# Optimization experiments

Measured on AMD Instinct MI355X. Metric: run time of the kernel, lower is better.

The kernel has to match this reference:

```python
import jax, jax.numpy as jnp
import numpy as np
from jax import lax

C = 512
B, T, N = 8, 16, 32
KSZ = 7
NEG_SLOPE = 0.01
LN_EPS = 1e-5


def setup_inputs() -> dict:
    key = jax.random.key(0)
    ks = jax.random.split(key, 8)
    local_feat = jax.random.normal(ks[0], (B, T, N, C), dtype=jnp.float32)
    global_feat = jax.random.normal(ks[1], (B, C), dtype=jnp.float32)
    pos = jax.random.normal(ks[2], (B, T, N, 3), dtype=jnp.float32)
    # adj_weight: nn.Linear(C, C, bias=False), init eye_ (perturb slightly to keep interesting ties)
    W = jnp.eye(C, dtype=jnp.float32) + 0.01 * jax.random.normal(ks[3], (C, C), dtype=jnp.float32)
    # depthwise Conv1d(C, C, 7, groups=C): weight [C, 1, 7], kaiming init; bias zeros
    conv_w = jax.random.normal(ks[4], (C, 1, KSZ), dtype=jnp.float32) * np.sqrt(2.0 / KSZ)
    conv_b = jnp.zeros((C,), dtype=jnp.float32)
    ln_gamma = jnp.ones((C,), dtype=jnp.float32)
    ln_beta = jnp.zeros((C,), dtype=jnp.float32)
    return {"local_feat": local_feat, "global_feat": global_feat, "pos": pos,
            "W": W, "conv_w": conv_w, "conv_b": conv_b,
            "ln_gamma": ln_gamma, "ln_beta": ln_beta}


def reference(local_feat, global_feat, pos, W, conv_w, conv_b, ln_gamma, ln_beta):
    b, t, nd, c = local_feat.shape
    n = t * nd
    feat = local_feat.reshape(b, n, c)
    # F.normalize(p=2, dim=-1, eps=1e-12)
    norm = feat / jnp.maximum(jnp.linalg.norm(feat, axis=-1, keepdims=True), 1e-12)
    # torch.einsum('bnc,cc,bcm->bnm'): repeated 'cc' takes the diagonal of W
    A = jnp.einsum('bnc,cc,bcm->bnm', norm, W, jnp.swapaxes(norm, 1, 2))
    A = A.reshape(b, n, t, nd)
    top_A = jnp.argmax(A, axis=-1)  # [b, n, t]
    # direct indexed gather -- avoids the [b, n, t, nd, c] stacked blowup
    top_feat = local_feat[jnp.arange(b)[:, None, None],
                          jnp.arange(t)[None, None, :],
                          top_A]                                 # [b, n, t, c]
    x = jnp.swapaxes(top_feat.reshape(b * n, t, c), 1, 2)        # [b*n, c, t]
    # depthwise conv1d, kernel 7, valid padding
    y = lax.conv_general_dilated(x, conv_w, window_strides=(1,), padding='VALID',
                                 dimension_numbers=('NCH', 'OIH', 'NCH'),
                                 feature_group_count=c)
    y = y + conv_b[None, :, None]                                # [b*n, c, t-6]
    y = jnp.swapaxes(y, 1, 2)                                    # [b*n, t-6, c]
    mu = jnp.mean(y, axis=-1, keepdims=True)
    var = jnp.mean(jnp.square(y - mu), axis=-1, keepdims=True)
    ln = (y - mu) * lax.rsqrt(var + LN_EPS) * ln_gamma + ln_beta
    act = jnp.where(ln >= 0, ln, NEG_SLOPE * ln)
    out = jnp.mean(act, axis=1)                                  # mean over time -> [b*n, c]
    return out.reshape(b, t, nd, c)
```

## Files before the change

### kernel.cpp

```cpp
#include <hip/hip_runtime.h>
#include <hip/hip_bf16.h>

#define C_DIM 512
#define B_DIM 8
#define T_DIM 16
#define ND_DIM 32
#define NPTS 512
#define ROWS 4096
#define KSZ 7
#define TOUT 10
#define NEG_SLOPE 0.01f
#define LN_EPS 1e-5f

__global__ __launch_bounds__(256) void norm_kernel(const float* __restrict__ feat,
                                                   float* __restrict__ nrm) {
    int row = blockIdx.x;
    int tid = threadIdx.x;
    const float* f = feat + (size_t)row * C_DIM;
    float* o = nrm + (size_t)row * C_DIM;
    float v0 = f[tid];
    float v1 = f[tid + 256];
    float ss = v0 * v0 + v1 * v1;
    #pragma unroll
    for (int off = 32; off > 0; off >>= 1) ss += __shfl_down(ss, off, 64);
    __shared__ float wsum[4];
    int wid = tid >> 6, lane = tid & 63;
    if (lane == 0) wsum[wid] = ss;
    __syncthreads();
    float tot = wsum[0] + wsum[1] + wsum[2] + wsum[3];
    float inv = 1.0f / fmaxf(sqrtf(tot), 1e-12f);
    o[tid] = v0 * inv;
    o[tid + 256] = v1 * inv;
}

__global__ __launch_bounds__(256) void gemm_argmax_kernel(const float* __restrict__ nrm,
                                                          const float* __restrict__ W,
                                                          int* __restrict__ idxg) {
    __shared__ __align__(16) float As[16][68];
    __shared__ __align__(16) float Bs[16][68];
    __shared__ float Cs[64][65];
    __shared__ float wd[C_DIM];
    const int tid = threadIdx.x;
    const int tx = tid & 15, ty = tid >> 4;
    const int b = blockIdx.z;
    const int row0 = blockIdx.y * 64, col0 = blockIdx.x * 64;
    const float* Nb = nrm + (size_t)b * NPTS * C_DIM;

    wd[tid]       = W[(size_t)tid * (C_DIM + 1)];
    wd[tid + 256] = W[(size_t)(tid + 256) * (C_DIM + 1)];
    __syncthreads();

    float acc[4][4] = {};
    for (int k0 = 0; k0 < C_DIM; k0 += 16) {
        #pragma unroll
        for (int e = 0; e < 4; e++) {
            int idx = tid + e * 256;
            int m = idx >> 4, kk = idx & 15;
            As[kk][m] = Nb[(size_t)(row0 + m) * C_DIM + k0 + kk] * wd[k0 + kk];
            Bs[kk][m] = Nb[(size_t)(col0 + m) * C_DIM + k0 + kk];
        }
        __syncthreads();
        #pragma unroll
        for (int kk = 0; kk < 16; kk++) {
            float4 a4 = *(const float4*)&As[kk][ty * 4];
            float4 b4 = *(const float4*)&Bs[kk][tx * 4];
            float av[4] = {a4.x, a4.y, a4.z, a4.w};
            float bv[4] = {b4.x, b4.y, b4.z, b4.w};
            #pragma unroll
            for (int i = 0; i < 4; i++)
                #pragma unroll
                for (int j = 0; j < 4; j++)
                    acc[i][j] += av[i] * bv[j];
        }
        __syncthreads();
    }

    #pragma unroll
    for (int i = 0; i < 4; i++)
        #pragma unroll
        for (int j = 0; j < 4; j++)
            Cs[ty * 4 + i][tx * 4 + j] = acc[i][j];
    __syncthreads();
    if (tid < 128) {
        int r = tid >> 1, g = tid & 1;
        const float* crow = &Cs[r][g * 32];
        float best = crow[0];
        int bi = 0;
        for (int j = 1; j < 32; j++) {
            float v = crow[j];
            if (v > best) { best = v; bi = j; }
        }
        int n_glob = b * NPTS + row0 + r;
        int tg = (col0 >> 5) + g;
        idxg[(size_t)n_glob * T_DIM + tg] = bi;
    }
}

__global__ __launch_bounds__(256, 2) void fuse_kernel(const int* __restrict__ idxg,
                                                      const float* __restrict__ lf,
                                                      const float* __restrict__ cw,
                                                      const float* __restrict__ cb,
                                                      const float* __restrict__ gamma,
                                                      const float* __restrict__ beta,
                                                      float* __restrict__ out) {
    const int wave = threadIdx.x >> 6;
    const int lane = threadIdx.x & 63;
    const int bn = blockIdx.x * 4 + wave;
    const int b = bn >> 9;
    const int c0 = lane * 8;

    float x[T_DIM][8];
    #pragma unroll
    for (int t = 0; t < T_DIM; t++) {
        int idx = idxg[(size_t)bn * T_DIM + t];
        const float* p = lf + (((size_t)(b * T_DIM + t)) * ND_DIM + idx) * C_DIM + c0;
        float4 lo = *(const float4*)p;
        float4 hi = *(const float4*)(p + 4);
        x[t][0] = lo.x; x[t][1] = lo.y; x[t][2] = lo.z; x[t][3] = lo.w;
        x[t][4] = hi.x; x[t][5] = hi.y; x[t][6] = hi.z; x[t][7] = hi.w;
    }

    float w[KSZ][8];
    #pragma unroll
    for (int c = 0; c < 8; c++)
        #pragma unroll
        for (int k = 0; k < KSZ; k++)
            w[k][c] = cw[(size_t)(c0 + c) * KSZ + k];
    float bias[8], g[8], be[8];
    {
        float4 b_lo = *(const float4*)&cb[c0],    b_hi = *(const float4*)&cb[c0 + 4];
        float4 g_lo = *(const float4*)&gamma[c0], g_hi = *(const float4*)&gamma[c0 + 4];
        float4 e_lo = *(const float4*)&beta[c0],  e_hi = *(const float4*)&beta[c0 + 4];
        bias[0]=b_lo.x; bias[1]=b_lo.y; bias[2]=b_lo.z; bias[3]=b_lo.w;
        bias[4]=b_hi.x; bias[5]=b_hi.y; bias[6]=b_hi.z; bias[7]=b_hi.w;
        g[0]=g_lo.x; g[1]=g_lo.y; g[2]=g_lo.z; g[3]=g_lo.w;
        g[4]=g_hi.x; g[5]=g_hi.y; g[6]=g_hi.z; g[7]=g_hi.w;
        be[0]=e_lo.x; be[1]=e_lo.y; be[2]=e_lo.z; be[3]=e_lo.w;
        be[4]=e_hi.x; be[5]=e_hi.y; be[6]=e_hi.z; be[7]=e_hi.w;
    }

    float accum[8] = {};
    #pragma unroll
    for (int tau = 0; tau < TOUT; tau++) {
        float y[8];
        #pragma unroll
        for (int c = 0; c < 8; c++) {
            float v = bias[c];
            #pragma unroll
            for (int k = 0; k < KSZ; k++) v += x[tau + k][c] * w[k][c];
            y[c] = v;
        }
        float s = 0.f, q = 0.f;
        #pragma unroll
        for (int c = 0; c < 8; c++) { s += y[c]; q += y[c] * y[c]; }
        #pragma unroll
        for (int m = 1; m < 64; m <<= 1) {
            s += __shfl_xor(s, m, 64);
            q += __shfl_xor(q, m, 64);
        }
        float mu = s * (1.0f / 512.0f);
        float var = q * (1.0f / 512.0f) - mu * mu;
        float rs = rsqrtf(var + LN_EPS);
        #pragma unroll
        for (int c = 0; c < 8; c++) {
            float ln = (y[c] - mu) * rs * g[c] + be[c];
            accum[c] += ln >= 0.f ? ln : NEG_SLOPE * ln;
        }
    }
    float* o = out + (size_t)bn * C_DIM + c0;
    float4 r_lo = make_float4(accum[0]*0.1f, accum[1]*0.1f, accum[2]*0.1f, accum[3]*0.1f);
    float4 r_hi = make_float4(accum[4]*0.1f, accum[5]*0.1f, accum[6]*0.1f, accum[7]*0.1f);
    *(float4*)o = r_lo;
    *(float4*)(o + 4) = r_hi;
}

__global__ void sentinel_kernel(float* out, int n, float val) {
    int i = blockIdx.x * 256 + threadIdx.x;
    if (i < n) out[i] = val;
}

extern "C" void kernel_launch(void* const* d_in, const int* in_sizes, int n_in,
                              void* d_out, int out_size, void* d_ws, size_t ws_size,
                              hipStream_t stream) {
    const float* local_feat = (const float*)d_in[0];
    const float* W       = (const float*)d_in[3];
    const float* conv_w  = (const float*)d_in[4];
    const float* conv_b  = (const float*)d_in[5];
    const float* ln_g    = (const float*)d_in[6];
    const float* ln_b    = (const float*)d_in[7];
    float* out = (float*)d_out;

    (void)hipGetLastError();

    const size_t nrm_bytes = (size_t)ROWS * C_DIM * sizeof(float);
    const size_t idx_bytes = (size_t)ROWS * T_DIM * sizeof(int);
    if (d_ws == nullptr || ws_size < nrm_bytes + idx_bytes) {
        float val = 512.0f + (float)(ws_size >> 20);
        sentinel_kernel<<<(out_size + 255) / 256, 256, 0, stream>>>(out, out_size, val);
        return;
    }

    float* nrm = (float*)d_ws;
    int* idxg  = (int*)((char*)d_ws + nrm_bytes);

    norm_kernel<<<ROWS, 256, 0, stream>>>(local_feat, nrm);

    gemm_argmax_kernel<<<dim3(NPTS / 64, NPTS / 64, B_DIM), 256, 0, stream>>>(nrm, W, idxg);

    fuse_kernel<<<ROWS / 4, 256, 0, stream>>>(idxg, local_feat, conv_w, conv_b,
                                              ln_g, ln_b, out);

    if (hipGetLastError() != hipSuccess) {
        hipMemsetAsync(d_out, 0x42, (size_t)out_size * 2, stream);
    }
}
```

Measured before the change: 136.4 us.

## Split-K 128x128 double-buffered GEMM with separate reduce-argmax kernel

Replaces the 64x64 fused GEMM+argmax with a 128x128 register-tiled (8x8 per thread) GEMM. The GEMM splits K in two and double-buffers shared memory with vectorized float4 loads. Partial results go to workspace and a new kernel sums both halves and does the per-group argmax with wave shuffles. This raises arithmetic intensity and keeps enough blocks in flight, at the cost of writing and reading 16 MB of partial sums and one extra launch. The new path runs only when the workspace is large enough.

New measurement: 150.7 us. 10.5% more time.

```diff
diff --git a/kernel.cpp b/kernel.cpp
--- a/kernel.cpp
+++ b/kernel.cpp
@@ -31,6 +31,103 @@
     float inv = 1.0f / fmaxf(sqrtf(tot), 1e-12f);
     o[tid] = v0 * inv;
     o[tid + 256] = v1 * inv;
+}
+
+__global__ __launch_bounds__(256, 1) void gemm_part_kernel(const float* __restrict__ nrm,
+                                                           const float* __restrict__ W,
+                                                           float* __restrict__ part) {
+    __shared__ __align__(16) float As[2][128][20];
+    __shared__ __align__(16) float Bs[2][128][20];
+    __shared__ float wd[256];
+    const int tid = threadIdx.x;
+    const int tx = tid & 15, ty = tid >> 4;
+    const int b = blockIdx.z >> 1, kz = blockIdx.z & 1;
+    const int row0 = blockIdx.y * 128, col0 = blockIdx.x * 128;
+    const int kbase = kz * 256;
+    const float* __restrict__ Nb = nrm + (size_t)b * NPTS * C_DIM;
+
+    wd[tid] = W[(size_t)(kbase + tid) * (C_DIM + 1)];
+    __syncthreads();
+
+    const int sr = tid >> 1;
+    const int kh = (tid & 1) * 8;
+
+    {
+        const float* ga = Nb + (size_t)(row0 + sr) * C_DIM + kbase + kh;
+        const float* gb = Nb + (size_t)(col0 + sr) * C_DIM + kbase + kh;
+        float4 a0 = *(const float4*)ga, a1 = *(const float4*)(ga + 4);
+        float4 b0 = *(const float4*)gb, b1 = *(const float4*)(gb + 4);
+        float4 w0 = *(const float4*)&wd[kh], w1 = *(const float4*)&wd[kh + 4];
+        a0.x *= w0.x; a0.y *= w0.y; a0.z *= w0.z; a0.w *= w0.w;
+        a1.x *= w1.x; a1.y *= w1.y; a1.z *= w1.z; a1.w *= w1.w;
+        *(float4*)&As[0][sr][kh] = a0; *(float4*)&As[0][sr][kh + 4] = a1;
+        *(float4*)&Bs[0][sr][kh] = b0; *(float4*)&Bs[0][sr][kh + 4] = b1;
+    }
+
+    float acc[8][8] = {};
+    #pragma unroll 1
+    for (int step = 0; step < 16; ++step) {
+        __syncthreads();
+        const int buf = step & 1;
+        if (step + 1 < 16) {
+            const int koff = (step + 1) * 16;
+            const float* ga = Nb + (size_t)(row0 + sr) * C_DIM + kbase + koff + kh;
+            const float* gb = Nb + (size_t)(col0 + sr) * C_DIM + kbase + koff + kh;
+            float4 a0 = *(const float4*)ga, a1 = *(const float4*)(ga + 4);
+            float4 b0 = *(const float4*)gb, b1 = *(const float4*)(gb + 4);
+            float4 w0 = *(const float4*)&wd[koff + kh], w1 = *(const float4*)&wd[koff + kh + 4];
+            a0.x *= w0.x; a0.y *= w0.y; a0.z *= w0.z; a0.w *= w0.w;
+            a1.x *= w1.x; a1.y *= w1.y; a1.z *= w1.z; a1.w *= w1.w;
+            *(float4*)&As[buf ^ 1][sr][kh] = a0; *(float4*)&As[buf ^ 1][sr][kh + 4] = a1;
+            *(float4*)&Bs[buf ^ 1][sr][kh] = b0; *(float4*)&Bs[buf ^ 1][sr][kh + 4] = b1;
+        }
+        #pragma unroll
+        for (int k4 = 0; k4 < 4; ++k4) {
+            float4 av[8], bv[8];
+            #pragma unroll
+            for (int i = 0; i < 8; i++) av[i] = *(const float4*)&As[buf][ty + 16 * i][k4 * 4];
+            #pragma unroll
+            for (int j = 0; j < 8; j++) bv[j] = *(const float4*)&Bs[buf][tx + 16 * j][k4 * 4];
+            #pragma unroll
+            for (int i = 0; i < 8; i++)
+                #pragma unroll
+                for (int j = 0; j < 8; j++)
+                    acc[i][j] += av[i].x * bv[j].x + av[i].y * bv[j].y
+                               + av[i].z * bv[j].z + av[i].w * bv[j].w;
+        }
+    }
+
+    float* Cb = part + ((size_t)(kz * B_DIM + b) * NPTS + row0) * NPTS + col0;
+    #pragma unroll
+    for (int i = 0; i < 8; i++)
+        #pragma unroll
+        for (int j = 0; j < 8; j++)
+            Cb[(size_t)(ty + 16 * i) * NPTS + tx + 16 * j] = acc[i][j];
+}
+
+__global__ __launch_bounds__(256) void reduce_argmax_kernel(const float* __restrict__ part,
+                                                            int* __restrict__ idxg) {
+    const int bn = blockIdx.x * 4 + (threadIdx.x >> 6);
+    const int lane = threadIdx.x & 63;
+    const float* p0 = part + (size_t)bn * NPTS + lane * 8;
+    const float* p1 = part + (size_t)(ROWS + bn) * NPTS + lane * 8;
+    float4 x0 = *(const float4*)p0, x1 = *(const float4*)(p0 + 4);
+    float4 y0 = *(const float4*)p1, y1 = *(const float4*)(p1 + 4);
+    float v[8] = { x0.x + y0.x, x0.y + y0.y, x0.z + y0.z, x0.w + y0.w,
+                   x1.x + y1.x, x1.y + y1.y, x1.z + y1.z, x1.w + y1.w };
+    float best = v[0];
+    int bc = lane * 8;
+    #pragma unroll
+    for (int c = 1; c < 8; c++) {
+        if (v[c] > best) { best = v[c]; bc = lane * 8 + c; }
+    }
+    #pragma unroll
+    for (int m = 1; m < 4; m <<= 1) {
+        float ov = __shfl_xor(best, m, 64);
+        int oc = __shfl_xor(bc, m, 64);
+        if (ov > best || (ov == best && oc < bc)) { best = ov; bc = oc; }
+    }
+    if ((lane & 3) == 0) idxg[(size_t)bn * T_DIM + (lane >> 2)] = bc & 31;
 }
 
 __global__ __launch_bounds__(256) void gemm_argmax_kernel(const float* __restrict__ nrm,
@@ -74,7 +171,6 @@
         }
         __syncthreads();
     }
-
     #pragma unroll
     for (int i = 0; i < 4; i++)
         #pragma unroll
@@ -192,8 +288,10 @@
 
     (void)hipGetLastError();
 
-    const size_t nrm_bytes = (size_t)ROWS * C_DIM * sizeof(float);
-    const size_t idx_bytes = (size_t)ROWS * T_DIM * sizeof(int);
+    const size_t nrm_bytes  = (size_t)ROWS * C_DIM * sizeof(float);
+    const size_t part_bytes = (size_t)2 * ROWS * NPTS * sizeof(float);
+    const size_t idx_bytes  = (size_t)ROWS * T_DIM * sizeof(int);
+
     if (d_ws == nullptr || ws_size < nrm_bytes + idx_bytes) {
         float val = 512.0f + (float)(ws_size >> 20);
         sentinel_kernel<<<(out_size + 255) / 256, 256, 0, stream>>>(out, out_size, val);
@@ -201,11 +299,19 @@
     }
 
     float* nrm = (float*)d_ws;
-    int* idxg  = (int*)((char*)d_ws + nrm_bytes);
 
     norm_kernel<<<ROWS, 256, 0, stream>>>(local_feat, nrm);
 
-    gemm_argmax_kernel<<<dim3(NPTS / 64, NPTS / 64, B_DIM), 256, 0, stream>>>(nrm, W, idxg);
+    int* idxg;
+    if (ws_size >= nrm_bytes + part_bytes + idx_bytes) {
+        float* part = (float*)((char*)d_ws + nrm_bytes);
+        idxg = (int*)((char*)d_ws + nrm_bytes + part_bytes);
+        gemm_part_kernel<<<dim3(NPTS / 128, NPTS / 128, B_DIM * 2), 256, 0, stream>>>(nrm, W, part);
+        reduce_argmax_kernel<<<ROWS / 4, 256, 0, stream>>>(part, idxg);
+    } else {
+        idxg = (int*)((char*)d_ws + nrm_bytes);
+        gemm_argmax_kernel<<<dim3(NPTS / 64, NPTS / 64, B_DIM), 256, 0, stream>>>(nrm, W, idxg);
+    }
 
     fuse_kernel<<<ROWS / 4, 256, 0, stream>>>(idxg, local_feat, conv_w, conv_b,
                                               ln_g, ln_b, out);
```
